# Performance work log

Measured on AMD Instinct MI355X. Metric: run time of the kernel, lower is better.

The kernel has to match this reference:

```python
import jax, jax.numpy as jnp
import numpy as np
from jax import lax


def _c1x1(t, w, b=None):
    # t: [B,C,H,W], w: [O,C] (1x1 conv == channel matmul)
    y = jnp.einsum('bchw,oc->bohw', t, w)
    if b is not None:
        y = y + b[None, :, None, None]
    return y


def _mamba(u, in_w, conv_w, conv_b, xproj_w, dt_w, dt_b, A_log, Dp, out_w):
    # u: [B,L,d_model]; Mamba block (mamba_ssm defaults: in/out/x_proj bias=False)
    B, L, _ = u.shape
    d_inner = conv_w.shape[0]
    d_state = A_log.shape[1]
    dt_rank = dt_w.shape[1]
    d_conv = conv_w.shape[2]
    xz = jnp.einsum('bld,ed->ble', u, in_w)          # [B,L,2*d_inner]
    xc, z = xz[..., :d_inner], xz[..., d_inner:]
    # depthwise causal conv1d over seq
    xt = jnp.pad(xc.transpose(0, 2, 1), ((0, 0), (0, 0), (d_conv - 1, 0)))
    xt = lax.conv_general_dilated(xt, conv_w, (1,), 'VALID',
                                  feature_group_count=d_inner,
                                  dimension_numbers=('NCH', 'OIH', 'NCH'))
    xc = jax.nn.silu(xt + conv_b[None, :, None]).transpose(0, 2, 1)  # [B,L,d_inner]
    dbc = jnp.einsum('bld,ed->ble', xc, xproj_w)     # [B,L,dt_rank+2*d_state]
    dt = dbc[..., :dt_rank]
    B_ = dbc[..., dt_rank:dt_rank + d_state]
    C_ = dbc[..., dt_rank + d_state:]
    delta = jax.nn.softplus(jnp.einsum('blr,dr->bld', dt, dt_w) + dt_b)  # [B,L,d_inner]
    A = -jnp.exp(A_log)                              # [d_inner,d_state]
    dA = jnp.exp(delta[..., None] * A)               # [B,L,D,N]
    dBu = delta[..., None] * B_[:, :, None, :] * xc[..., None]
    def step(h, inp):
        dA_t, dBu_t, c_t = inp
        h = dA_t * h + dBu_t                         # [B,D,N]
        y = jnp.einsum('bdn,bn->bd', h, c_t)
        return h, y
    h0 = jnp.zeros((B, d_inner, d_state), dtype=u.dtype)
    _, ys = lax.scan(step, h0, (dA.transpose(1, 0, 2, 3),
                                dBu.transpose(1, 0, 2, 3),
                                C_.transpose(1, 0, 2)))
    y = ys.transpose(1, 0, 2) + xc * Dp              # [B,L,d_inner]
    y = y * jax.nn.silu(z)
    return jnp.einsum('bld,od->blo', y, out_w)       # [B,L,d_model]


def setup_inputs() -> dict:
    key = jax.random.key(0)
    B, C, H, W = 8, 128, 160, 160
    mip, d_in, d_st, d_r, d_cv = 8, 256, 16, 8, 4
    ks = iter(jax.random.split(key, 64))
    def rn(shape, s=0.05):
        return (jax.random.normal(next(ks), shape, dtype=jnp.float32) * s)
    inp = {'x': jax.random.normal(next(ks), (B, C, H, W), dtype=jnp.float32)}
    inp.update(conv1_w=rn((mip, C)), conv1_b=rn((mip,)),
               bn_g=jnp.ones((mip,)), bn_b=jnp.zeros((mip,)),
               bn_m=jnp.zeros((mip,)), bn_v=jnp.ones((mip,)),
               convh_w=rn((C, mip)), convh_b=rn((C,)),
               convw_w=rn((C, mip)), convw_b=rn((C,)),
               mlpx_w1=rn((C, C)), mlpx_b1=rn((C,)), mlpx_w2=rn((C, C)), mlpx_b2=rn((C,)),
               mlpy_w1=rn((C, C)), mlpy_b1=rn((C,)), mlpy_w2=rn((C, C)), mlpy_b2=rn((C,)),
               adjust_w=rn((C, 2 * C)))
    for p in ('mx', 'my'):
        inp[p + '_in_w'] = rn((2 * d_in, C))
        inp[p + '_conv_w'] = rn((d_in, 1, d_cv), 0.3)
        inp[p + '_conv_b'] = rn((d_in,))
        inp[p + '_xproj_w'] = rn((d_r + 2 * d_st, d_in))
        inp[p + '_dt_w'] = rn((d_in, d_r))
        inp[p + '_dt_b'] = rn((d_in,))
        inp[p + '_Alog'] = jnp.log(jnp.broadcast_to(jnp.arange(1, d_st + 1, dtype=jnp.float32), (d_in, d_st)))
        inp[p + '_D'] = jnp.ones((d_in,))
        inp[p + '_out_w'] = rn((C, d_in))
    return inp


def reference(x, conv1_w, conv1_b, bn_g, bn_b, bn_m, bn_v, convh_w, convh_b,
              convw_w, convw_b, mlpx_w1, mlpx_b1, mlpx_w2, mlpx_b2,
              mlpy_w1, mlpy_b1, mlpy_w2, mlpy_b2, adjust_w,
              mx_in_w, mx_conv_w, mx_conv_b, mx_xproj_w, mx_dt_w, mx_dt_b,
              mx_Alog, mx_D, mx_out_w,
              my_in_w, my_conv_w, my_conv_b, my_xproj_w, my_dt_w, my_dt_b,
              my_Alog, my_D, my_out_w):
    B, C, H, W = x.shape
    gelu = lambda t: jax.nn.gelu(t, approximate=False)
    # CoordAttWithMLP
    x_h = x.mean(3, keepdims=True)                      # [B,C,H,1]
    x_w = x.mean(2, keepdims=True).transpose(0, 1, 3, 2)  # [B,C,W,1]
    y = jnp.concatenate([x_h, x_w], axis=2)             # [B,C,H+W,1]
    y = _c1x1(y, conv1_w, conv1_b)
    y = (y - bn_m[None, :, None, None]) * jax.lax.rsqrt(bn_v + 1e-5)[None, :, None, None]
    y = y * bn_g[None, :, None, None] + bn_b[None, :, None, None]
    y = gelu(y)
    a_h = _c1x1(y[:, :, :H], convh_w, convh_b)          # [B,C,H,1] (pre-sigmoid)
    a_w = _c1x1(y[:, :, H:].transpose(0, 1, 3, 2), convw_w, convw_b)  # [B,C,1,W]
    # EfficientMambaAttention00
    ux = x.mean(3).transpose(0, 2, 1)                   # [B,H,C]
    x_x = _mamba(ux, mx_in_w, mx_conv_w, mx_conv_b, mx_xproj_w,
                 mx_dt_w, mx_dt_b, mx_Alog, mx_D, mx_out_w)
    x_x = x_x.transpose(0, 2, 1)[..., None]             # [B,C,H,1]
    x_x = jax.nn.sigmoid(x_x + a_h)
    x_x = _c1x1(gelu(_c1x1(x_x, mlpx_w1, mlpx_b1)), mlpx_w2, mlpx_b2)
    uy = x.mean(2).transpose(0, 2, 1)                   # [B,W,C]
    x_y = _mamba(uy, my_in_w, my_conv_w, my_conv_b, my_xproj_w,
                 my_dt_w, my_dt_b, my_Alog, my_D, my_out_w)
    x_y = x_y.transpose(0, 2, 1)[:, :, None, :]         # [B,C,1,W]
    x_y = jax.nn.sigmoid(x_y + a_w)
    x_y = _c1x1(gelu(_c1x1(x_y, mlpy_w1, mlpy_b1)), mlpy_w2, mlpy_b2)
    # combine
    result_h = jax.nn.sigmoid(a_h) * x_y                # [B,C,H,W]
    result_w = jax.nn.sigmoid(a_w) * x_x                # [B,C,H,W]
    out1 = _c1x1(jnp.concatenate([result_h, result_w], axis=1), adjust_w)
    return x * out1
```

## Files before the change

### kernel.cpp

```cpp
#include <hip/hip_runtime.h>
#include <hip/hip_bf16.h>
#include <math.h>


typedef __attribute__((ext_vector_type(8))) short short8;
typedef __attribute__((ext_vector_type(4))) float f32x4;

__device__ __forceinline__ float sigm_(float x){ return 1.f/(1.f+__expf(-x)); }
__device__ __forceinline__ float silu_(float x){ return x/(1.f+__expf(-x)); }
__device__ __forceinline__ float gelu_(float x){ return 0.5f*x*(1.f+erff(x*0.7071067811865476f)); }
__device__ __forceinline__ float softplus_(float x){ return (x>20.f)?x:log1pf(__expf(x)); }

__global__ void k_means(const float* __restrict__ x, float* __restrict__ xh, float* __restrict__ xw){
  int bc = blockIdx.x;
  const float* xt = x + (size_t)bc*25600;
  int tid = threadIdx.x, wave = tid>>6, lane = tid&63;
  __shared__ float4 colpart[4][40];
  float csx=0.f, csy=0.f, csz=0.f, csw=0.f;
  for (int i=0;i<40;i++){
    int h = wave*40+i;
    float4 v = make_float4(0.f,0.f,0.f,0.f);
    if (lane<40) v = ((const float4*)(xt + h*160))[lane];
    csx+=v.x; csy+=v.y; csz+=v.z; csw+=v.w;
    float r = v.x+v.y+v.z+v.w;
    for (int off=32; off>0; off>>=1) r += __shfl_down(r, off, 64);
    if (lane==0) xh[(size_t)bc*160+h] = r*(1.f/160.f);
  }
  if (lane<40) colpart[wave][lane] = make_float4(csx,csy,csz,csw);
  __syncthreads();
  if (tid<40){
    float4 a=colpart[0][tid], b=colpart[1][tid], c=colpart[2][tid], d=colpart[3][tid];
    float4 s = make_float4((a.x+b.x+c.x+d.x)*(1.f/160.f), (a.y+b.y+c.y+d.y)*(1.f/160.f),
                           (a.z+b.z+c.z+d.z)*(1.f/160.f), (a.w+b.w+c.w+d.w)*(1.f/160.f));
    ((float4*)(xw + (size_t)bc*160))[tid] = s;
  }
}

__global__ void k_ybranch(const float* __restrict__ xh, const float* __restrict__ xw,
                          const float* __restrict__ w1, const float* __restrict__ b1,
                          const float* __restrict__ bg, const float* __restrict__ bb,
                          const float* __restrict__ bm, const float* __restrict__ bv,
                          float* __restrict__ ybuf){
  int gid = blockIdx.x*blockDim.x + threadIdx.x;
  if (gid >= 8*320) return;
  int b = gid/320, p = gid%320;
  const float* in = (p<160) ? (xh + (size_t)b*128*160 + p) : (xw + (size_t)b*128*160 + (p-160));
  float acc[8] = {0,0,0,0,0,0,0,0};
  for (int c=0;c<128;c++){
    float u = in[c*160];
    #pragma unroll
    for (int m=0;m<8;m++) acc[m] += w1[m*128+c]*u;
  }
  #pragma unroll
  for (int m=0;m<8;m++){
    float val = acc[m] + b1[m];
    val = (val - bm[m]) * rsqrtf(bv[m] + 1e-5f);
    val = val * bg[m] + bb[m];
    ybuf[(b*320+p)*8+m] = gelu_(val);
  }
}

__global__ void k_ahw(const float* __restrict__ ybuf,
                      const float* __restrict__ wh, const float* __restrict__ bh,
                      const float* __restrict__ ww, const float* __restrict__ bw,
                      float* __restrict__ a_h, float* __restrict__ a_w,
                      float* __restrict__ SHT, float* __restrict__ SW){
  int gid = blockIdx.x*blockDim.x + threadIdx.x;
  if (gid >= 8*128*320) return;
  int p = gid%320; int c = (gid/320)%128; int b = gid/(320*128);
  const float* yv = ybuf + (size_t)(b*320+p)*8;
  const float* w = (p<160)? (wh + c*8) : (ww + c*8);
  float acc = (p<160)? bh[c] : bw[c];
  #pragma unroll
  for (int m=0;m<8;m++) acc += w[m]*yv[m];
  if (p<160){
    size_t o = ((size_t)(b*128+c))*160+p;
    a_h[o] = acc;
    SHT[((size_t)(b*160+p))*128 + c] = sigm_(acc);
  } else {
    size_t o = ((size_t)(b*128+c))*160+(p-160);
    a_w[o] = acc; SW[o] = sigm_(acc);
  }
}

__global__ __launch_bounds__(256) void k_inproj(
                         const float* __restrict__ xh, const float* __restrict__ xw,
                         const float* __restrict__ inw0, const float* __restrict__ inw1,
                         float* __restrict__ xcpre, float* __restrict__ zb){
  __shared__ float uS[8][128];
  int blk = blockIdx.x;
  int g = blk/160, rem = blk%160, b = rem/20, lt = rem%20, lbase = lt*8;
  int t = threadIdx.x;
  const float* src = (g==0)? xh : xw;
  {
    int c = t>>1, lh = t&1;
    float4 v = *(const float4*)(src + ((size_t)(b*128+c))*160 + lbase + lh*4);
    uS[lh*4+0][c]=v.x; uS[lh*4+1][c]=v.y; uS[lh*4+2][c]=v.z; uS[lh*4+3][c]=v.w;
  }
  __syncthreads();
  const float* inw = (g==0)? inw0 : inw1;
  const float* w0p = inw + (size_t)t*128;
  const float* w1p = inw + (size_t)(t+256)*128;
  float acc0[8]={0,0,0,0,0,0,0,0}, acc1[8]={0,0,0,0,0,0,0,0};
  for (int ct=0; ct<16; ct++){
    float4 wa = *(const float4*)(w0p + ct*8);
    float4 wb = *(const float4*)(w0p + ct*8 + 4);
    float4 wc = *(const float4*)(w1p + ct*8);
    float4 wd = *(const float4*)(w1p + ct*8 + 4);
    #pragma unroll
    for (int l=0;l<8;l++){
      float4 ua = *(const float4*)&uS[l][ct*8];
      float4 ub = *(const float4*)&uS[l][ct*8+4];
      acc0[l] += wa.x*ua.x + wa.y*ua.y + wa.z*ua.z + wa.w*ua.w
               + wb.x*ub.x + wb.y*ub.y + wb.z*ub.z + wb.w*ub.w;
      acc1[l] += wc.x*ua.x + wc.y*ua.y + wc.z*ua.z + wc.w*ua.w
               + wd.x*ub.x + wd.y*ub.y + wd.z*ub.z + wd.w*ub.w;
    }
  }
  size_t ob = ((size_t)(g*8+b)*160 + lbase)*256;
  #pragma unroll
  for (int l=0;l<8;l++){
    xcpre[ob + (size_t)l*256 + t] = acc0[l];
    zb   [ob + (size_t)l*256 + t] = acc1[l];
  }
}

__global__ void k_conv(const float* __restrict__ xcpre,
                       const float* __restrict__ cw0, const float* __restrict__ cb0,
                       const float* __restrict__ cw1, const float* __restrict__ cb1,
                       float* __restrict__ xcb){
  int gid = blockIdx.x*blockDim.x + threadIdx.x;
  if (gid >= 2*8*160*256) return;
  int d = gid & 255; int t = gid >> 8; int l = t % 160; int gb = t / 160; int g = gb >> 3;
  const float* cw = ((g==0)? cw0 : cw1) + d*4;
  float acc = ((g==0)? cb0 : cb1)[d];
  const float* base = xcpre + (size_t)gb*160*256 + d;
  #pragma unroll
  for (int k=0;k<4;k++){
    int ls = l-3+k;
    if (ls>=0) acc += cw[k] * base[(size_t)ls*256];
  }
  xcb[gid] = silu_(acc);
}

__global__ void k_prep(const float* __restrict__ adjw, __hip_bfloat16* __restrict__ adjwb){
  int i = blockIdx.x*256 + threadIdx.x;
  if (i < 32768) adjwb[i] = __float2bfloat16(adjw[i]);
}

__global__ __launch_bounds__(256) void k_xproj(
                        const float* __restrict__ xcb,
                        const float* __restrict__ xp0, const float* __restrict__ xp1,
                        float* __restrict__ dbc){
  __shared__ float xv[32][260];
  int blk = blockIdx.x;
  int g = blk/40, rem = blk%40, b = rem/5, lt = rem%5, lbase = lt*32;
  int t = threadIdx.x;
  size_t base = ((size_t)(g*8+b)*160 + lbase)*256;
  for (int i=t; i<8192; i+=256){ int l=i>>8, d=i&255; xv[l][d] = xcb[base+i]; }
  __syncthreads();
  int l = t>>3, s = t&7;
  const float* xp = (g==0)? xp0 : xp1;
  size_t orow = ((size_t)(g*8+b)*160 + lbase + l)*40;
  for (int q=0;q<5;q++){
    int j = s + q*8;
    const float* w = xp + j*256;
    float acc=0.f;
    for (int dd=0; dd<256; dd+=8){
      float4 wa = *(const float4*)(w+dd);
      float4 wb = *(const float4*)(w+dd+4);
      float4 ua = *(const float4*)&xv[l][dd];
      float4 ub = *(const float4*)&xv[l][dd+4];
      acc += wa.x*ua.x + wa.y*ua.y + wa.z*ua.z + wa.w*ua.w
           + wb.x*ub.x + wb.y*ub.y + wb.z*ub.z + wb.w*ub.w;
    }
    dbc[orow + j] = acc;
  }
}

__global__ __launch_bounds__(256) void k_scan(
                       const float* __restrict__ dbc,
                       const float* __restrict__ xcb, const float* __restrict__ zb,
                       const float* __restrict__ dtw0, const float* __restrict__ dtb0,
                       const float* __restrict__ dtw1, const float* __restrict__ dtb1,
                       const float* __restrict__ Alog0, const float* __restrict__ Alog1,
                       const float* __restrict__ D0, const float* __restrict__ D1,
                       float* __restrict__ ysb){
  __shared__ float dsS[160][16];
  __shared__ float BS [160][16];
  __shared__ float CS [160][16];
  __shared__ float xcS[160][16];
  __shared__ float yS [160][16];
  int blk = blockIdx.x;
  int gb = blk >> 4, dblk = blk & 15, g = gb >> 3;
  int dbase = dblk*16;
  int t = threadIdx.x;
  size_t base = (size_t)gb*160*256;
  const float* db = dbc + (size_t)gb*6400;
  const float* dtwG = (g==0)? dtw0 : dtw1;
  const float* dtbG = (g==0)? dtb0 : dtb1;

  #pragma unroll
  for (int i=0;i<10;i++){
    int item = t + 256*i;
    int l = item>>4, c = item&15;
    const float* r = db + l*40;
    int d = dbase + c;
    const float* wt = dtwG + d*8;
    float4 w0 = *(const float4*)wt;
    float4 w1 = *(const float4*)(wt+4);
    float4 r0 = *(const float4*)r;
    float4 r1 = *(const float4*)(r+4);
    float dt = dtbG[d] + w0.x*r0.x+w0.y*r0.y+w0.z*r0.z+w0.w*r0.w
                       + w1.x*r1.x+w1.y*r1.y+w1.z*r1.z+w1.w*r1.w;
    dsS[l][c] = softplus_(dt);
    BS [l][c] = r[8+c];
    CS [l][c] = r[24+c];
    xcS[l][c] = xcb[base + (size_t)l*256 + dbase + c];
  }
  __syncthreads();

  int dloc = t>>4, n = t&15;
  int d = dbase + dloc;
  float A  = -__expf(((g==0)? Alog0 : Alog1)[d*16+n]);
  float Dd = ((g==0)? D0 : D1)[d];
  float h = 0.f;
  for (int lc=0; lc<160; lc+=8){
    float ds8[8], B8[8], C8[8], xc8[8];
    #pragma unroll
    for (int j=0;j<8;j++){
      ds8[j]=dsS[lc+j][dloc]; B8[j]=BS[lc+j][n];
      C8[j]=CS[lc+j][n];      xc8[j]=xcS[lc+j][dloc];
    }
    #pragma unroll
    for (int j=0;j<8;j++){
      float dA = __expf(ds8[j]*A);
      h = dA*h + ds8[j]*B8[j]*xc8[j];
      float p = h*C8[j];
      p += __shfl_xor(p,1,16); p += __shfl_xor(p,2,16);
      p += __shfl_xor(p,4,16); p += __shfl_xor(p,8,16);
      if (n==0) yS[lc+j][dloc] = p + xc8[j]*Dd;
    }
  }
  __syncthreads();

  #pragma unroll
  for (int i=0;i<10;i++){
    int item = t + 256*i;
    int l = item>>4, c = item&15;
    size_t gi = base + (size_t)l*256 + dbase + c;
    ysb[gi] = yS[l][c] * silu_(zb[gi]);
  }
}

__global__ __launch_bounds__(256) void k_post(
                       const float* __restrict__ ysb,
                       const float* __restrict__ ow0, const float* __restrict__ ow1,
                       const float* __restrict__ a_h, const float* __restrict__ a_w,
                       const float* __restrict__ w1x, const float* __restrict__ b1x,
                       const float* __restrict__ w1y, const float* __restrict__ b1y,
                       const float* __restrict__ w2x, const float* __restrict__ b2x,
                       const float* __restrict__ w2y, const float* __restrict__ b2y,
                       float* __restrict__ QxT, float* __restrict__ Qy){
  __shared__ float ysS[10][256];
  __shared__ float Sc[10][128];
  __shared__ float Sp[10][128];
  int blk = blockIdx.x;
  int g = blk>>7, rem = blk&127, b = rem>>4, lt = rem&15, lbase = lt*10;
  int t = threadIdx.x; int c = t&127, kh = t>>7;
  size_t ybase = ((size_t)(g*8+b)*160 + lbase)*256;
  for (int i=t; i<2560; i+=256) ((float*)ysS)[i] = ysb[ybase+i];
  __syncthreads();
  float acc[10];
  {
    const float* w = ((g==0)? ow0 : ow1) + (size_t)c*256 + kh*128;
    #pragma unroll
    for (int l=0;l<10;l++) acc[l]=0.f;
    for (int ct=0; ct<16; ct++){
      float4 wa = *(const float4*)(w + ct*8);
      float4 wb = *(const float4*)(w + ct*8 + 4);
      #pragma unroll
      for (int l=0;l<10;l++){
        float4 ua = *(const float4*)&ysS[l][kh*128+ct*8];
        float4 ub = *(const float4*)&ysS[l][kh*128+ct*8+4];
        acc[l] += wa.x*ua.x + wa.y*ua.y + wa.z*ua.z + wa.w*ua.w
                + wb.x*ub.x + wb.y*ub.y + wb.z*ub.z + wb.w*ub.w;
      }
    }
  }
  if (kh==1){ for (int l=0;l<10;l++) Sc[l][c] = acc[l]; }
  __syncthreads();
  if (kh==0){
    const float* a = ((g==0)? a_h : a_w) + ((size_t)(b*128+c))*160 + lbase;
    #pragma unroll
    for (int l=0;l<10;l++) Sp[l][c] = sigm_(acc[l] + Sc[l][c] + a[l]);
  }
  __syncthreads();
  {
    const float* w = ((g==0)? w1x : w1y) + (size_t)c*128 + kh*64;
    #pragma unroll
    for (int l=0;l<10;l++) acc[l]=0.f;
    for (int ct=0; ct<8; ct++){
      float4 wa = *(const float4*)(w + ct*8);
      float4 wb = *(const float4*)(w + ct*8 + 4);
      #pragma unroll
      for (int l=0;l<10;l++){
        float4 ua = *(const float4*)&Sp[l][kh*64+ct*8];
        float4 ub = *(const float4*)&Sp[l][kh*64+ct*8+4];
        acc[l] += wa.x*ua.x + wa.y*ua.y + wa.z*ua.z + wa.w*ua.w
                + wb.x*ub.x + wb.y*ub.y + wb.z*ub.z + wb.w*ub.w;
      }
    }
  }
  if (kh==1){ for (int l=0;l<10;l++) Sc[l][c] = acc[l]; }
  __syncthreads();
  if (kh==0){
    float bb = ((g==0)? b1x : b1y)[c];
    float tv[10];
    #pragma unroll
    for (int l=0;l<10;l++) tv[l] = gelu_(bb + acc[l] + Sc[l][c]);
    __syncthreads();
    #pragma unroll
    for (int l=0;l<10;l++) Sp[l][c] = tv[l];
  } else {
    __syncthreads();
  }
  __syncthreads();
  {
    const float* w = ((g==0)? w2x : w2y) + (size_t)c*128 + kh*64;
    #pragma unroll
    for (int l=0;l<10;l++) acc[l]=0.f;
    for (int ct=0; ct<8; ct++){
      float4 wa = *(const float4*)(w + ct*8);
      float4 wb = *(const float4*)(w + ct*8 + 4);
      #pragma unroll
      for (int l=0;l<10;l++){
        float4 ua = *(const float4*)&Sp[l][kh*64+ct*8];
        float4 ub = *(const float4*)&Sp[l][kh*64+ct*8+4];
        acc[l] += wa.x*ua.x + wa.y*ua.y + wa.z*ua.z + wa.w*ua.w
                + wb.x*ub.x + wb.y*ub.y + wb.z*ub.z + wb.w*ub.w;
      }
    }
  }
  if (kh==1){ for (int l=0;l<10;l++) Sc[l][c] = acc[l]; }
  __syncthreads();
  if (kh==0){
    float bb = ((g==0)? b2x : b2y)[c];
    if (g==0){
      #pragma unroll
      for (int l=0;l<10;l++)
        QxT[((size_t)(b*160 + lbase + l))*128 + c] = bb + acc[l] + Sc[l][c];
    } else {
      size_t orow = ((size_t)(b*128+c))*160 + lbase;
      #pragma unroll
      for (int l=0;l<10;l++) Qy[orow + l] = bb + acc[l] + Sc[l][c];
    }
  }
}

__global__ __launch_bounds__(256) void k_final_mfma(
                       const float* __restrict__ x,
                       const float* __restrict__ SHT, const float* __restrict__ SW,
                       const float* __restrict__ QxT, const float* __restrict__ Qy,
                       const __hip_bfloat16* __restrict__ adjwb, float* __restrict__ out){
  __shared__ __hip_bfloat16 F[80*136];
  int blk0 = blockIdx.x;
  int blk = (blk0 & 7)*320 + (blk0 >> 3);
  int b = blk/320; int rem = blk%320; int h = rem>>1; int wh = rem&1;
  int wbase = wh*80;
  int tid = threadIdx.x;
  int kq = tid & 127, whh = tid >> 7;
  int wid = tid>>6, lane = tid&63, quad = lane>>4, l16 = lane&15;

  float s0 = SHT[((size_t)(b*160+h))*128 + kq];
  float s1 = QxT[((size_t)(b*160+h))*128 + kq];

  size_t prow = ((size_t)(b*128+kq))*160 + wbase + whh*40;
  const float4* rp0 = (const float4*)(Qy + prow);
  const float4* rp1 = (const float4*)(SW + prow);

  float4 v0[10], v1[10];
  #pragma unroll
  for (int u=0;u<10;u++) v0[u] = rp0[u];
  #pragma unroll
  for (int u=0;u<10;u++) v1[u] = rp1[u];
  #pragma unroll
  for (int u=0;u<10;u++){
    int wr = whh*40 + u*4;
    F[(wr+0)*136 + kq] = __float2bfloat16(s0*v0[u].x);
    F[(wr+1)*136 + kq] = __float2bfloat16(s0*v0[u].y);
    F[(wr+2)*136 + kq] = __float2bfloat16(s0*v0[u].z);
    F[(wr+3)*136 + kq] = __float2bfloat16(s0*v0[u].w);
  }
  __syncthreads();

  f32x4 acc[2][5];
  #pragma unroll
  for (int i=0;i<2;i++)
    #pragma unroll
    for (int nt=0;nt<5;nt++) acc[i][nt] = (f32x4){0.f,0.f,0.f,0.f};

  {
    short8 bfrag[2][4];
    #pragma unroll
    for (int i=0;i<2;i++){
      const __hip_bfloat16* bp = adjwb + (size_t)((wid*2+i)*16 + l16)*256 + quad*8;
      #pragma unroll
      for (int kc=0;kc<4;kc++) bfrag[i][kc] = *(const short8*)(bp + kc*32);
    }
    #pragma unroll
    for (int nt=0; nt<5; nt++){
      const __hip_bfloat16* ap = &F[(nt*16 + l16)*136 + quad*8];
      #pragma unroll
      for (int kc=0;kc<4;kc++){
        short8 af = *(const short8*)(ap + kc*32);
        acc[0][nt] = __builtin_amdgcn_mfma_f32_16x16x32_bf16(af, bfrag[0][kc], acc[0][nt], 0,0,0);
        acc[1][nt] = __builtin_amdgcn_mfma_f32_16x16x32_bf16(af, bfrag[1][kc], acc[1][nt], 0,0,0);
      }
    }
  }
  __syncthreads();

  #pragma unroll
  for (int u=0;u<10;u++){
    int wr = whh*40 + u*4;
    F[(wr+0)*136 + kq] = __float2bfloat16(s1*v1[u].x);
    F[(wr+1)*136 + kq] = __float2bfloat16(s1*v1[u].y);
    F[(wr+2)*136 + kq] = __float2bfloat16(s1*v1[u].z);
    F[(wr+3)*136 + kq] = __float2bfloat16(s1*v1[u].w);
  }
  float4 xv[2][5];
  size_t rbA = (((size_t)(b*128 + (wid*2+0)*16 + l16))*160 + h)*160 + wbase + quad*4;
  size_t rbB = (((size_t)(b*128 + (wid*2+1)*16 + l16))*160 + h)*160 + wbase + quad*4;
  #pragma unroll
  for (int nt=0;nt<5;nt++){
    xv[0][nt] = *(const float4*)(x + rbA + nt*16);
    xv[1][nt] = *(const float4*)(x + rbB + nt*16);
  }
  __syncthreads();

  {
    short8 bfrag[2][4];
    #pragma unroll
    for (int i=0;i<2;i++){
      const __hip_bfloat16* bp = adjwb + (size_t)((wid*2+i)*16 + l16)*256 + 128 + quad*8;
      #pragma unroll
      for (int kc=0;kc<4;kc++) bfrag[i][kc] = *(const short8*)(bp + kc*32);
    }
    #pragma unroll
    for (int nt=0; nt<5; nt++){
      const __hip_bfloat16* ap = &F[(nt*16 + l16)*136 + quad*8];
      #pragma unroll
      for (int kc=0;kc<4;kc++){
        short8 af = *(const short8*)(ap + kc*32);
        acc[0][nt] = __builtin_amdgcn_mfma_f32_16x16x32_bf16(af, bfrag[0][kc], acc[0][nt], 0,0,0);
        acc[1][nt] = __builtin_amdgcn_mfma_f32_16x16x32_bf16(af, bfrag[1][kc], acc[1][nt], 0,0,0);
      }
    }
  }

  #pragma unroll
  for (int i=0;i<2;i++){
    size_t rb = i? rbB : rbA;
    #pragma unroll
    for (int nt=0; nt<5; nt++){
      f32x4 a = acc[i][nt];
      float4 xvv = xv[i][nt];
      f32x4 ov = (f32x4){xvv.x*a[0], xvv.y*a[1], xvv.z*a[2], xvv.w*a[3]};
      __builtin_nontemporal_store(ov, (f32x4*)(out + rb + nt*16));
    }
  }
}

extern "C" void kernel_launch(void* const* d_in, const int* in_sizes, int n_in,
                              void* d_out, int out_size, void* d_ws, size_t ws_size,
                              hipStream_t stream) {
  #define W(i) ((const float*)d_in[i])
  const float* X = W(0);
  float* ws = (float*)d_ws;
  float* xh    = ws;
  float* xw    = xh    + 163840;
  float* ybuf  = xw    + 163840;
  float* ah    = ybuf  + 20480;
  float* aw    = ah    + 163840;
  float* xcpre = aw    + 163840;
  float* zb    = xcpre + 655360;
  float* xcb   = zb    + 655360;
  float* dbc   = xcb   + 655360;
  float* ysb   = dbc   + 102400;
  float* QxT   = ysb   + 655360;
  float* Qy    = QxT   + 163840;
  __hip_bfloat16* adjwb = (__hip_bfloat16*)xcpre;
  float* SHT   = xcpre + 16384;
  float* SW    = SHT   + 163840;

  k_means  <<<1024, 256, 0, stream>>>(X, xh, xw);
  k_ybranch<<<10,   256, 0, stream>>>(xh, xw, W(1), W(2), W(3), W(4), W(5), W(6), ybuf);
  k_inproj <<<320,  256, 0, stream>>>(xh, xw, W(20), W(29), xcpre, zb);
  k_conv   <<<2560, 256, 0, stream>>>(xcpre, W(21), W(22), W(30), W(31), xcb);
  k_prep   <<<128,  256, 0, stream>>>(W(19), adjwb);
  k_ahw    <<<1280, 256, 0, stream>>>(ybuf, W(7), W(8), W(9), W(10), ah, aw, SHT, SW);
  k_xproj  <<<80,   256, 0, stream>>>(xcb, W(23), W(32), dbc);
  k_scan   <<<256,  256, 0, stream>>>(dbc, xcb, zb, W(24), W(25), W(33), W(34),
                                      W(26), W(35), W(27), W(36), ysb);
  k_post   <<<256,  256, 0, stream>>>(ysb, W(28), W(37), ah, aw,
                                      W(11), W(12), W(15), W(16),
                                      W(13), W(14), W(17), W(18), QxT, Qy);
  k_final_mfma<<<2560, 256, 0, stream>>>(X, SHT, SW, QxT, Qy, adjwb, (float*)d_out);
  #undef W
}
```

Before: 458.2 us.

## Process five rows per block in final GEMM, double-buffer F, fuse weight prep

The final MFMA kernel now handles five consecutive h rows per block, so Qy/SW rows are loaded once and reused across all five. The LDS tile is double-buffered so the next F build can overlap the current MFMA. The grid shrinks from 2560 to 512 blocks and launch bounds ask for two blocks per CU. The adjust-weight bf16 conversion is folded into k_ahw as extra blocks, removing one launch. Output stores switch from nontemporal to regular, and fewer blocks with more registers risk lower occupancy and parallelism.

```diff
diff --git a/kernel.cpp b/kernel.cpp
--- a/kernel.cpp
+++ b/kernel.cpp
@@ -64,9 +64,15 @@
                       const float* __restrict__ wh, const float* __restrict__ bh,
                       const float* __restrict__ ww, const float* __restrict__ bw,
                       float* __restrict__ a_h, float* __restrict__ a_w,
-                      float* __restrict__ SHT, float* __restrict__ SW){
-  int gid = blockIdx.x*blockDim.x + threadIdx.x;
-  if (gid >= 8*128*320) return;
+                      float* __restrict__ SHT, float* __restrict__ SW,
+                      const float* __restrict__ adjw, __hip_bfloat16* __restrict__ adjwb){
+  int blk = blockIdx.x;
+  if (blk >= 1280){
+    int i = (blk-1280)*256 + threadIdx.x;
+    if (i < 32768) adjwb[i] = __float2bfloat16(adjw[i]);
+    return;
+  }
+  int gid = blk*256 + threadIdx.x;
   int p = gid%320; int c = (gid/320)%128; int b = gid/(320*128);
   const float* yv = ybuf + (size_t)(b*320+p)*8;
   const float* w = (p<160)? (wh + c*8) : (ww + c*8);
@@ -141,11 +147,6 @@
     if (ls>=0) acc += cw[k] * base[(size_t)ls*256];
   }
   xcb[gid] = silu_(acc);
-}
-
-__global__ void k_prep(const float* __restrict__ adjw, __hip_bfloat16* __restrict__ adjwb){
-  int i = blockIdx.x*256 + threadIdx.x;
-  if (i < 32768) adjwb[i] = __float2bfloat16(adjw[i]);
 }
 
 __global__ __launch_bounds__(256) void k_xproj(
@@ -358,117 +359,124 @@
   }
 }
 
-__global__ __launch_bounds__(256) void k_final_mfma(
+__device__ __forceinline__ void build_F(__hip_bfloat16* Fb, float s, const float4* v,
+                                        int whh, int kq){
+  #pragma unroll
+  for (int u=0;u<10;u++){
+    int wr = whh*40 + u*4;
+    Fb[(wr+0)*136 + kq] = __float2bfloat16(s*v[u].x);
+    Fb[(wr+1)*136 + kq] = __float2bfloat16(s*v[u].y);
+    Fb[(wr+2)*136 + kq] = __float2bfloat16(s*v[u].z);
+    Fb[(wr+3)*136 + kq] = __float2bfloat16(s*v[u].w);
+  }
+}
+
+__global__ __launch_bounds__(256,2) void k_final_mfma(
                        const float* __restrict__ x,
                        const float* __restrict__ SHT, const float* __restrict__ SW,
                        const float* __restrict__ QxT, const float* __restrict__ Qy,
                        const __hip_bfloat16* __restrict__ adjwb, float* __restrict__ out){
-  __shared__ __hip_bfloat16 F[80*136];
+  __shared__ __hip_bfloat16 F[2][80*136];
   int blk0 = blockIdx.x;
-  int blk = (blk0 & 7)*320 + (blk0 >> 3);
-  int b = blk/320; int rem = blk%320; int h = rem>>1; int wh = rem&1;
+  int b = blk0 & 7, inner = blk0 >> 3;
+  int ht = inner >> 1, wh = inner & 1;
+  int h0 = ht*5;
   int wbase = wh*80;
   int tid = threadIdx.x;
   int kq = tid & 127, whh = tid >> 7;
   int wid = tid>>6, lane = tid&63, quad = lane>>4, l16 = lane&15;
 
-  float s0 = SHT[((size_t)(b*160+h))*128 + kq];
-  float s1 = QxT[((size_t)(b*160+h))*128 + kq];
-
+  float s0[5], s1[5];
+  #pragma unroll
+  for (int j=0;j<5;j++){
+    s0[j] = SHT[((size_t)(b*160+h0+j))*128 + kq];
+    s1[j] = QxT[((size_t)(b*160+h0+j))*128 + kq];
+  }
   size_t prow = ((size_t)(b*128+kq))*160 + wbase + whh*40;
   const float4* rp0 = (const float4*)(Qy + prow);
   const float4* rp1 = (const float4*)(SW + prow);
-
   float4 v0[10], v1[10];
   #pragma unroll
   for (int u=0;u<10;u++) v0[u] = rp0[u];
   #pragma unroll
   for (int u=0;u<10;u++) v1[u] = rp1[u];
-  #pragma unroll
-  for (int u=0;u<10;u++){
-    int wr = whh*40 + u*4;
-    F[(wr+0)*136 + kq] = __float2bfloat16(s0*v0[u].x);
-    F[(wr+1)*136 + kq] = __float2bfloat16(s0*v0[u].y);
-    F[(wr+2)*136 + kq] = __float2bfloat16(s0*v0[u].z);
-    F[(wr+3)*136 + kq] = __float2bfloat16(s0*v0[u].w);
-  }
-  __syncthreads();
-
-  f32x4 acc[2][5];
-  #pragma unroll
-  for (int i=0;i<2;i++)
-    #pragma unroll
-    for (int nt=0;nt<5;nt++) acc[i][nt] = (f32x4){0.f,0.f,0.f,0.f};
-
-  {
-    short8 bfrag[2][4];
+
+  build_F(F[0], s0[0], v0, whh, kq);
+  __syncthreads();
+
+  size_t rowA = ((size_t)(b*128 + (wid*2+0)*16 + l16))*25600 + wbase + quad*4;
+  size_t rowB = ((size_t)(b*128 + (wid*2+1)*16 + l16))*25600 + wbase + quad*4;
+
+  #pragma unroll
+  for (int j=0;j<5;j++){
+    int h = h0 + j;
+    float4 xv[2][5];
+    #pragma unroll
+    for (int nt=0;nt<5;nt++){
+      xv[0][nt] = *(const float4*)(x + rowA + (size_t)h*160 + nt*16);
+      xv[1][nt] = *(const float4*)(x + rowB + (size_t)h*160 + nt*16);
+    }
+    f32x4 acc[2][5];
+    #pragma unroll
+    for (int i=0;i<2;i++)
+      #pragma unroll
+      for (int nt=0;nt<5;nt++) acc[i][nt] = (f32x4){0.f,0.f,0.f,0.f};
+
+    {
+      short8 bf[2][4];
+      #pragma unroll
+      for (int i=0;i<2;i++){
+        const __hip_bfloat16* bp = adjwb + (size_t)((wid*2+i)*16 + l16)*256 + quad*8;
+        #pragma unroll
+        for (int kc=0;kc<4;kc++) bf[i][kc] = *(const short8*)(bp + kc*32);
+      }
+      #pragma unroll
+      for (int nt=0; nt<5; nt++){
+        const __hip_bfloat16* ap = &F[0][(nt*16 + l16)*136 + quad*8];
+        #pragma unroll
+        for (int kc=0;kc<4;kc++){
+          short8 af = *(const short8*)(ap + kc*32);
+          acc[0][nt] = __builtin_amdgcn_mfma_f32_16x16x32_bf16(af, bf[0][kc], acc[0][nt], 0,0,0);
+          acc[1][nt] = __builtin_amdgcn_mfma_f32_16x16x32_bf16(af, bf[1][kc], acc[1][nt], 0,0,0);
+        }
+      }
+    }
+    build_F(F[1], s1[j], v1, whh, kq);
+    __syncthreads();
+
+    {
+      short8 bf[2][4];
+      #pragma unroll
+      for (int i=0;i<2;i++){
+        const __hip_bfloat16* bp = adjwb + (size_t)((wid*2+i)*16 + l16)*256 + 128 + quad*8;
+        #pragma unroll
+        for (int kc=0;kc<4;kc++) bf[i][kc] = *(const short8*)(bp + kc*32);
+      }
+      #pragma unroll
+      for (int nt=0; nt<5; nt++){
+        const __hip_bfloat16* ap = &F[1][(nt*16 + l16)*136 + quad*8];
+        #pragma unroll
+        for (int kc=0;kc<4;kc++){
+          short8 af = *(const short8*)(ap + kc*32);
+          acc[0][nt] = __builtin_amdgcn_mfma_f32_16x16x32_bf16(af, bf[0][kc], acc[0][nt], 0,0,0);
+          acc[1][nt] = __builtin_amdgcn_mfma_f32_16x16x32_bf16(af, bf[1][kc], acc[1][nt], 0,0,0);
+        }
+      }
+    }
+    if (j<4) build_F(F[0], s0[j+1], v0, whh, kq);
+
     #pragma unroll
     for (int i=0;i<2;i++){
-      const __hip_bfloat16* bp = adjwb + (size_t)((wid*2+i)*16 + l16)*256 + quad*8;
-      #pragma unroll
-      for (int kc=0;kc<4;kc++) bfrag[i][kc] = *(const short8*)(bp + kc*32);
-    }
-    #pragma unroll
-    for (int nt=0; nt<5; nt++){
-      const __hip_bfloat16* ap = &F[(nt*16 + l16)*136 + quad*8];
-      #pragma unroll
-      for (int kc=0;kc<4;kc++){
-        short8 af = *(const short8*)(ap + kc*32);
-        acc[0][nt] = __builtin_amdgcn_mfma_f32_16x16x32_bf16(af, bfrag[0][kc], acc[0][nt], 0,0,0);
-        acc[1][nt] = __builtin_amdgcn_mfma_f32_16x16x32_bf16(af, bfrag[1][kc], acc[1][nt], 0,0,0);
-      }
-    }
-  }
-  __syncthreads();
-
-  #pragma unroll
-  for (int u=0;u<10;u++){
-    int wr = whh*40 + u*4;
-    F[(wr+0)*136 + kq] = __float2bfloat16(s1*v1[u].x);
-    F[(wr+1)*136 + kq] = __float2bfloat16(s1*v1[u].y);
-    F[(wr+2)*136 + kq] = __float2bfloat16(s1*v1[u].z);
-    F[(wr+3)*136 + kq] = __float2bfloat16(s1*v1[u].w);
-  }
-  float4 xv[2][5];
-  size_t rbA = (((size_t)(b*128 + (wid*2+0)*16 + l16))*160 + h)*160 + wbase + quad*4;
-  size_t rbB = (((size_t)(b*128 + (wid*2+1)*16 + l16))*160 + h)*160 + wbase + quad*4;
-  #pragma unroll
-  for (int nt=0;nt<5;nt++){
-    xv[0][nt] = *(const float4*)(x + rbA + nt*16);
-    xv[1][nt] = *(const float4*)(x + rbB + nt*16);
-  }
-  __syncthreads();
-
-  {
-    short8 bfrag[2][4];
-    #pragma unroll
-    for (int i=0;i<2;i++){
-      const __hip_bfloat16* bp = adjwb + (size_t)((wid*2+i)*16 + l16)*256 + 128 + quad*8;
-      #pragma unroll
-      for (int kc=0;kc<4;kc++) bfrag[i][kc] = *(const short8*)(bp + kc*32);
-    }
-    #pragma unroll
-    for (int nt=0; nt<5; nt++){
-      const __hip_bfloat16* ap = &F[(nt*16 + l16)*136 + quad*8];
-      #pragma unroll
-      for (int kc=0;kc<4;kc++){
-        short8 af = *(const short8*)(ap + kc*32);
-        acc[0][nt] = __builtin_amdgcn_mfma_f32_16x16x32_bf16(af, bfrag[0][kc], acc[0][nt], 0,0,0);
-        acc[1][nt] = __builtin_amdgcn_mfma_f32_16x16x32_bf16(af, bfrag[1][kc], acc[1][nt], 0,0,0);
-      }
-    }
-  }
-
-  #pragma unroll
-  for (int i=0;i<2;i++){
-    size_t rb = i? rbB : rbA;
-    #pragma unroll
-    for (int nt=0; nt<5; nt++){
-      f32x4 a = acc[i][nt];
-      float4 xvv = xv[i][nt];
-      f32x4 ov = (f32x4){xvv.x*a[0], xvv.y*a[1], xvv.z*a[2], xvv.w*a[3]};
-      __builtin_nontemporal_store(ov, (f32x4*)(out + rb + nt*16));
-    }
+      size_t rb = (i? rowB : rowA) + (size_t)h*160;
+      #pragma unroll
+      for (int nt=0; nt<5; nt++){
+        f32x4 a = acc[i][nt];
+        float4 xvv = xv[i][nt];
+        float4 ov = make_float4(xvv.x*a[0], xvv.y*a[1], xvv.z*a[2], xvv.w*a[3]);
+        *(float4*)(out + rb + nt*16) = ov;
+      }
+    }
+    __syncthreads();
   }
 }
 
@@ -498,14 +506,14 @@
   k_ybranch<<<10,   256, 0, stream>>>(xh, xw, W(1), W(2), W(3), W(4), W(5), W(6), ybuf);
   k_inproj <<<320,  256, 0, stream>>>(xh, xw, W(20), W(29), xcpre, zb);
   k_conv   <<<2560, 256, 0, stream>>>(xcpre, W(21), W(22), W(30), W(31), xcb);
-  k_prep   <<<128,  256, 0, stream>>>(W(19), adjwb);
-  k_ahw    <<<1280, 256, 0, stream>>>(ybuf, W(7), W(8), W(9), W(10), ah, aw, SHT, SW);
+  k_ahw    <<<1408, 256, 0, stream>>>(ybuf, W(7), W(8), W(9), W(10), ah, aw, SHT, SW,
+                                      W(19), adjwb);
   k_xproj  <<<80,   256, 0, stream>>>(xcb, W(23), W(32), dbc);
   k_scan   <<<256,  256, 0, stream>>>(dbc, xcb, zb, W(24), W(25), W(33), W(34),
                                       W(26), W(35), W(27), W(36), ysb);
   k_post   <<<256,  256, 0, stream>>>(ysb, W(28), W(37), ah, aw,
                                       W(11), W(12), W(15), W(16),
                                       W(13), W(14), W(17), W(18), QxT, Qy);
-  k_final_mfma<<<2560, 256, 0, stream>>>(X, SHT, SW, QxT, Qy, adjwb, (float*)d_out);
+  k_final_mfma<<<512, 256, 0, stream>>>(X, SHT, SW, QxT, Qy, adjwb, (float*)d_out);
   #undef W
 }
```

Measured after the change: 458.1 us. Within noise of the previous version (-0.0%).
